# Optimization experiments

Measured on AMD Instinct MI355X. Metric: run time of the kernel, lower is better.

## Reference

```python
import jax, jax.numpy as jnp
import numpy as np

D_MODEL = 512
N_HEADS = 8
B, S = 4, 1024
REL_HIDDEN = 64


def setup_inputs() -> dict:
    key = jax.random.key(0)
    ks = jax.random.split(key, 16)

    def g(k, shape, scale=0.02):
        return jax.random.normal(k, shape, dtype=jnp.float32) * scale

    x = jax.random.normal(ks[0], (B, S, D_MODEL), dtype=jnp.float32)
    freqs = jax.random.uniform(ks[1], (B, S, 1), dtype=jnp.float32)
    return {
        "x": x,
        "freqs": freqs,
        "Wq": g(ks[2], (D_MODEL, D_MODEL)), "bq": g(ks[3], (D_MODEL,)),
        "Wk": g(ks[4], (D_MODEL, D_MODEL)), "bk": g(ks[5], (D_MODEL,)),
        "Wv": g(ks[6], (D_MODEL, D_MODEL)), "bv": g(ks[7], (D_MODEL,)),
        "Wo": g(ks[8], (D_MODEL, D_MODEL)), "bo": g(ks[9], (D_MODEL,)),
        "W1": g(ks[10], (2, REL_HIDDEN)), "b1": g(ks[11], (REL_HIDDEN,)),
        "W2": g(ks[12], (REL_HIDDEN, N_HEADS)), "b2": g(ks[13], (N_HEADS,)),
    }


def reference(x, freqs, Wq, bq, Wk, bk, Wv, bv, Wo, bo, W1, b1, W2, b2):
    b, s, d = x.shape
    h = N_HEADS
    dh = d // h

    def proj(W, bias):  # (b,s,d) -> (b,h,s,dh)
        return (x @ W + bias).reshape(b, s, h, dh).transpose(0, 2, 1, 3)

    Q = proj(Wq, bq)
    K = proj(Wk, bk)
    V = proj(Wv, bv)

    scores = jnp.einsum('bhid,bhjd->bhij', Q, K) / jnp.sqrt(jnp.float32(dh))

    # per-pair relative-frequency features: (b,s,s,2)
    eps = 1e-6
    fd = freqs[:, :, None, :] - freqs[:, None, :, :]
    fr = jnp.log((freqs[:, :, None, :] + eps) / (freqs[:, None, :, :] + eps))
    rel = jnp.concatenate([fd, fr], axis=-1)

    # MLP bias -> (b,s,s,h) -> (b,h,s,s)
    bias = jax.nn.relu(rel @ W1 + b1) @ W2 + b2
    scores = scores + jnp.transpose(bias, (0, 3, 1, 2))

    attn = jax.nn.softmax(scores, axis=-1)
    ctx = jnp.einsum('bhij,bhjd->bhid', attn, V)
    ctx = ctx.transpose(0, 2, 1, 3).reshape(b, s, d)
    return ctx @ Wo + bo
```

## Files before the change

### kernel.cpp

```cpp
#include <hip/hip_runtime.h>
#include <hip/hip_bf16.h>
#include <cstdint>

#define BATCH   4
#define SEQ     1024
#define DM      512
#define NH      8
#define DH      64
#define RH      64

typedef float f32x4 __attribute__((ext_vector_type(4)));
typedef __bf16 bf16x8 __attribute__((ext_vector_type(8)));

#define QB_OFF    (0)
#define KB_OFF    (4  << 20)
#define VT_OFF    (8  << 20)
#define XB_OFF    (12 << 20)
#define WT_OFF    (16 << 20)
#define WOT_OFF   (18 << 20)
#define W2T_OFF   (19 << 20)
#define AW_OFF    (20 << 20)
#define CW_OFF    (21 << 20)
#define CTXB_OFF  (22 << 20)
#define BIAS_OFF  (32 << 20)

__global__ __launch_bounds__(256) void cast_x(
    const float* __restrict__ x, __bf16* __restrict__ xb)
{
    const size_t i = ((size_t)blockIdx.x * 256 + threadIdx.x) * 8;
    const float4 a = *(const float4*)&x[i];
    const float4 b = *(const float4*)&x[i + 4];
    bf16x8 o;
    o[0] = (__bf16)a.x; o[1] = (__bf16)a.y; o[2] = (__bf16)a.z; o[3] = (__bf16)a.w;
    o[4] = (__bf16)b.x; o[5] = (__bf16)b.y; o[6] = (__bf16)b.z; o[7] = (__bf16)b.w;
    *(bf16x8*)&xb[i] = o;
}

__global__ __launch_bounds__(256) void cast_w(
    const float* __restrict__ Wq, const float* __restrict__ Wk,
    const float* __restrict__ Wv, const float* __restrict__ Wo,
    __bf16* __restrict__ Wt, __bf16* __restrict__ Wot)
{
    const int t = threadIdx.x;
    const int k0 = blockIdx.x * 64;
    const int n0 = blockIdx.y * 64;
    const int z  = blockIdx.z;
    const float* __restrict__ src = (z == 0) ? Wq : (z == 1) ? Wk : (z == 2) ? Wv : Wo;
    __bf16* __restrict__ dst = (z < 3) ? (Wt + (size_t)(z * 512 + n0) * 512)
                                       : (Wot + (size_t)n0 * 512);

    __shared__ __align__(16) float Ts[64][65];
    #pragma unroll
    for (int i = 0; i < 4; ++i) {
        const int id = t + i * 256;
        const int row = id >> 4, c4 = (id & 15) * 4;
        const float4 v = *(const float4*)&src[(size_t)(k0 + row) * DM + n0 + c4];
        Ts[row][c4 + 0] = v.x; Ts[row][c4 + 1] = v.y;
        Ts[row][c4 + 2] = v.z; Ts[row][c4 + 3] = v.w;
    }
    __syncthreads();
    #pragma unroll
    for (int i = 0; i < 2; ++i) {
        const int id = t + i * 256;
        const int rn = id >> 3, ck = (id & 7) * 8;
        bf16x8 o;
        #pragma unroll
        for (int j = 0; j < 8; ++j) o[j] = (__bf16)Ts[ck + j][rn];
        *(bf16x8*)&dst[(size_t)rn * 512 + k0 + ck] = o;
    }
}

__global__ __launch_bounds__(256) void gemm_qkv_mfma(
    const __bf16* __restrict__ xb, const __bf16* __restrict__ Wt,
    const float* __restrict__ bq, const float* __restrict__ bk,
    const float* __restrict__ bv,
    __bf16* __restrict__ Qb, __bf16* __restrict__ Kb, __bf16* __restrict__ Vtb)
{
    const int t = threadIdx.x;
    const int wave = t >> 6, lane = t & 63;
    const int wm = wave >> 1, wn = wave & 1;
    const int r = lane & 15, kc = lane >> 4, q4 = kc * 4;
    const int lin = blockIdx.y * 12 + blockIdx.x;
    const int swz = (lin & 7) * 48 + (lin >> 3);
    const int m0 = (swz / 12) * 128;
    const int n0 = (swz % 12) * 128;
    const int sec = n0 >> 9;
    const int nn = n0 & 511;

    __shared__ __align__(16) char smem[36864];
    __bf16* __restrict__ As = (__bf16*)smem;
    __bf16* __restrict__ Bs = (__bf16*)(smem + 18432);

    f32x4 acc[4][4];
    #pragma unroll
    for (int i = 0; i < 4; ++i)
        #pragma unroll
        for (int j = 0; j < 4; ++j) acc[i][j] = {0.f, 0.f, 0.f, 0.f};

    const int srow = t >> 3, sck = (t & 7) * 8;
    const __bf16* __restrict__ Ag = xb + (size_t)(m0 + srow) * 512 + sck;
    const __bf16* __restrict__ Bg = Wt + (size_t)(n0 + srow) * 512 + sck;

    for (int k0 = 0; k0 < 512; k0 += 64) {
        bf16x8 ra[4], rb[4];
        #pragma unroll
        for (int i = 0; i < 4; ++i) {
            ra[i] = *(const bf16x8*)(Ag + (size_t)i * 32 * 512 + k0);
            rb[i] = *(const bf16x8*)(Bg + (size_t)i * 32 * 512 + k0);
        }
        __syncthreads();
        #pragma unroll
        for (int i = 0; i < 4; ++i) {
            *(bf16x8*)&As[(srow + i * 32) * 72 + sck] = ra[i];
            *(bf16x8*)&Bs[(srow + i * 32) * 72 + sck] = rb[i];
        }
        __syncthreads();
        #pragma unroll
        for (int ks = 0; ks < 2; ++ks) {
            bf16x8 af[4], bf[4];
            #pragma unroll
            for (int mf = 0; mf < 4; ++mf)
                af[mf] = *(const bf16x8*)&As[(wm * 64 + mf * 16 + r) * 72 + ks * 32 + kc * 8];
            #pragma unroll
            for (int nf = 0; nf < 4; ++nf)
                bf[nf] = *(const bf16x8*)&Bs[(wn * 64 + nf * 16 + r) * 72 + ks * 32 + kc * 8];
            #pragma unroll
            for (int mf = 0; mf < 4; ++mf)
                #pragma unroll
                for (int nf = 0; nf < 4; ++nf)
                    acc[mf][nf] = __builtin_amdgcn_mfma_f32_16x16x32_bf16(
                        af[mf], bf[nf], acc[mf][nf], 0, 0, 0);
        }
    }

    const float* __restrict__ bias = (sec == 0) ? bq : (sec == 1) ? bk : bv;
    __syncthreads();
    __bf16* __restrict__ Ls = (__bf16*)smem;
    if (sec < 2) {
        #pragma unroll
        for (int mf = 0; mf < 4; ++mf)
            #pragma unroll
            for (int nf = 0; nf < 4; ++nf) {
                const int n_l = wn * 64 + nf * 16 + r;
                const float bb = bias[nn + n_l];
                #pragma unroll
                for (int rr = 0; rr < 4; ++rr)
                    Ls[(wm * 64 + mf * 16 + q4 + rr) * 136 + n_l] =
                        (__bf16)(acc[mf][nf][rr] + bb);
            }
    } else {
        #pragma unroll
        for (int mf = 0; mf < 4; ++mf)
            #pragma unroll
            for (int nf = 0; nf < 4; ++nf) {
                const int n_l = wn * 64 + nf * 16 + r;
                const float bb = bias[nn + n_l];
                #pragma unroll
                for (int rr = 0; rr < 4; ++rr)
                    Ls[n_l * 136 + (wm * 64 + mf * 16 + q4 + rr)] =
                        (__bf16)(acc[mf][nf][rr] + bb);
            }
    }
    __syncthreads();

    const int b = m0 >> 10, sbase = m0 & 1023;
    if (sec < 2) {
        __bf16* __restrict__ dst = sec ? Kb : Qb;
        #pragma unroll
        for (int i = 0; i < 8; ++i) {
            const int id = t + i * 256;
            const int row = id >> 4, nc = (id & 15) * 8;
            const bf16x8 v = *(const bf16x8*)&Ls[row * 136 + nc];
            const int ng = nn + nc, h = ng >> 6, c = ng & 63;
            *(bf16x8*)&dst[((size_t)(b * NH + h) * SEQ + sbase + row) * DH + c] = v;
        }
    } else {
        #pragma unroll
        for (int i = 0; i < 8; ++i) {
            const int id = t + i * 256;
            const int nrow = id >> 4, mc = (id & 15) * 8;
            const bf16x8 v = *(const bf16x8*)&Ls[nrow * 136 + mc];
            const int ng = nn + nrow, h = ng >> 6, c = ng & 63;
            *(bf16x8*)&Vtb[((size_t)(b * NH + h) * DH + c) * SEQ + sbase + mc] = v;
        }
    }
}

__global__ __launch_bounds__(256) void gemm_out_mfma(
    const __bf16* __restrict__ ctxb, const __bf16* __restrict__ Wot,
    const float* __restrict__ bo, float* __restrict__ out)
{
    const int t = threadIdx.x;
    const int wave = t >> 6, lane = t & 63;
    const int wm = wave >> 1, wn = wave & 1;
    const int r = lane & 15, kc = lane >> 4, q4 = kc * 4;
    const int lin = blockIdx.y * 4 + blockIdx.x;
    const int swz = (lin & 7) * 16 + (lin >> 3);
    const int m0 = (swz / 4) * 128;
    const int n0 = (swz % 4) * 128;

    __shared__ __align__(16) char smem[36864];
    __bf16* __restrict__ As = (__bf16*)smem;
    __bf16* __restrict__ Bs = (__bf16*)(smem + 18432);

    f32x4 acc[4][4];
    #pragma unroll
    for (int i = 0; i < 4; ++i)
        #pragma unroll
        for (int j = 0; j < 4; ++j) acc[i][j] = {0.f, 0.f, 0.f, 0.f};

    const int srow = t >> 3, sck = (t & 7) * 8;
    const __bf16* __restrict__ Ag = ctxb + (size_t)(m0 + srow) * 512 + sck;
    const __bf16* __restrict__ Bg = Wot + (size_t)(n0 + srow) * 512 + sck;

    for (int k0 = 0; k0 < 512; k0 += 64) {
        bf16x8 ra[4], rb[4];
        #pragma unroll
        for (int i = 0; i < 4; ++i) {
            ra[i] = *(const bf16x8*)(Ag + (size_t)i * 32 * 512 + k0);
            rb[i] = *(const bf16x8*)(Bg + (size_t)i * 32 * 512 + k0);
        }
        __syncthreads();
        #pragma unroll
        for (int i = 0; i < 4; ++i) {
            *(bf16x8*)&As[(srow + i * 32) * 72 + sck] = ra[i];
            *(bf16x8*)&Bs[(srow + i * 32) * 72 + sck] = rb[i];
        }
        __syncthreads();
        #pragma unroll
        for (int ks = 0; ks < 2; ++ks) {
            bf16x8 af[4], bf[4];
            #pragma unroll
            for (int mf = 0; mf < 4; ++mf)
                af[mf] = *(const bf16x8*)&As[(wm * 64 + mf * 16 + r) * 72 + ks * 32 + kc * 8];
            #pragma unroll
            for (int nf = 0; nf < 4; ++nf)
                bf[nf] = *(const bf16x8*)&Bs[(wn * 64 + nf * 16 + r) * 72 + ks * 32 + kc * 8];
            #pragma unroll
            for (int mf = 0; mf < 4; ++mf)
                #pragma unroll
                for (int nf = 0; nf < 4; ++nf)
                    acc[mf][nf] = __builtin_amdgcn_mfma_f32_16x16x32_bf16(
                        af[mf], bf[nf], acc[mf][nf], 0, 0, 0);
        }
    }

    #pragma unroll
    for (int mf = 0; mf < 4; ++mf)
        #pragma unroll
        for (int nf = 0; nf < 4; ++nf) {
            const int n_l = wn * 64 + nf * 16 + r;
            const float bb = bo[n0 + n_l];
            #pragma unroll
            for (int rr = 0; rr < 4; ++rr)
                out[(size_t)(m0 + wm * 64 + mf * 16 + q4 + rr) * DM + n0 + n_l] =
                    acc[mf][nf][rr] + bb;
        }
}

__global__ __launch_bounds__(64) void rel_kernel(
    const float* __restrict__ freqs,
    const float* __restrict__ W1,
    const float* __restrict__ b1,
    const float* __restrict__ W2,
    float* __restrict__ Aw,
    float* __restrict__ Cw,
    __bf16* __restrict__ W2t)
{
    const int row = blockIdx.x;
    const int k = threadIdx.x;
    const float f = freqs[row];
    const float L = logf(f + 1e-6f);
    const float base = f * W1[k] + L * W1[RH + k];
    Aw[(size_t)row * RH + k] = base + b1[k];
    Cw[(size_t)row * RH + k] = -base;
    if (row < 16)
        W2t[row * 64 + k] = (row < NH) ? (__bf16)W2[k * NH + row] : (__bf16)0.f;
}

__global__ __launch_bounds__(256) void bias_mfma(
    const float* __restrict__ Aw, const float* __restrict__ Cw,
    const __bf16* __restrict__ W2t, __bf16* __restrict__ biasb)
{
    const int t = threadIdx.x;
    const int wave = t >> 6, lane = t & 63;
    const int il = lane & 15, kc = lane >> 4;
    const int j0 = blockIdx.x * 128;
    const int i0 = blockIdx.y * 32;
    const int b  = blockIdx.z;

    __shared__ __align__(16) float Cs[128][68];

    {
        const int jr = t >> 1, half = (t & 1) * 32;
        const float* __restrict__ src = &Cw[((size_t)b * SEQ + j0 + jr) * RH + half];
        #pragma unroll
        for (int q = 0; q < 8; ++q)
            *(float4*)&Cs[jr][half + q * 4] = *(const float4*)(src + q * 4);
    }

    const bf16x8 w2f0 = *(const bf16x8*)&W2t[il * 64 + kc * 8];
    const bf16x8 w2f1 = *(const bf16x8*)&W2t[il * 64 + 32 + kc * 8];
    __syncthreads();

    #pragma unroll
    for (int ih = 0; ih < 2; ++ih) {
        const float* __restrict__ ap =
            &Aw[((size_t)b * SEQ + i0 + ih * 16 + il) * RH];
        const float4 a0 = *(const float4*)(ap + kc * 8);
        const float4 a1 = *(const float4*)(ap + kc * 8 + 4);
        const float4 a2 = *(const float4*)(ap + 32 + kc * 8);
        const float4 a3 = *(const float4*)(ap + 32 + kc * 8 + 4);

        #pragma unroll
        for (int jb = 0; jb < 4; ++jb) {
            f32x4 accJ[8];
            #pragma unroll
            for (int jj = 0; jj < 8; ++jj) {
                const float* __restrict__ cp =
                    &Cs[wave * 32 + jb * 8 + jj][kc * 8];
                const float4 c0 = *(const float4*)(cp);
                const float4 c1 = *(const float4*)(cp + 4);
                const float4 c2 = *(const float4*)(cp + 32);
                const float4 c3 = *(const float4*)(cp + 36);
                bf16x8 hb0, hb1;
                hb0[0] = (__bf16)fmaxf(a0.x + c0.x, 0.f);
                hb0[1] = (__bf16)fmaxf(a0.y + c0.y, 0.f);
                hb0[2] = (__bf16)fmaxf(a0.z + c0.z, 0.f);
                hb0[3] = (__bf16)fmaxf(a0.w + c0.w, 0.f);
                hb0[4] = (__bf16)fmaxf(a1.x + c1.x, 0.f);
                hb0[5] = (__bf16)fmaxf(a1.y + c1.y, 0.f);
                hb0[6] = (__bf16)fmaxf(a1.z + c1.z, 0.f);
                hb0[7] = (__bf16)fmaxf(a1.w + c1.w, 0.f);
                hb1[0] = (__bf16)fmaxf(a2.x + c2.x, 0.f);
                hb1[1] = (__bf16)fmaxf(a2.y + c2.y, 0.f);
                hb1[2] = (__bf16)fmaxf(a2.z + c2.z, 0.f);
                hb1[3] = (__bf16)fmaxf(a2.w + c2.w, 0.f);
                hb1[4] = (__bf16)fmaxf(a3.x + c3.x, 0.f);
                hb1[5] = (__bf16)fmaxf(a3.y + c3.y, 0.f);
                hb1[6] = (__bf16)fmaxf(a3.z + c3.z, 0.f);
                hb1[7] = (__bf16)fmaxf(a3.w + c3.w, 0.f);
                f32x4 acc = {0.f, 0.f, 0.f, 0.f};
                acc = __builtin_amdgcn_mfma_f32_16x16x32_bf16(hb0, w2f0, acc, 0, 0, 0);
                acc = __builtin_amdgcn_mfma_f32_16x16x32_bf16(hb1, w2f1, acc, 0, 0, 0);
                accJ[jj] = acc;
            }
            if (il < 8) {
                #pragma unroll
                for (int rr = 0; rr < 4; ++rr) {
                    bf16x8 pv;
                    #pragma unroll
                    for (int jj = 0; jj < 8; ++jj)
                        pv[jj] = (__bf16)accJ[jj][rr];
                    *(bf16x8*)&biasb[(((size_t)b * NH + il) * SEQ
                                      + i0 + ih * 16 + kc * 4 + rr) * SEQ
                                     + j0 + wave * 32 + jb * 8] = pv;
                }
            }
        }
    }
}

#define PSTR 1032

__global__ __launch_bounds__(512) void attn_mfma(
    const __bf16* __restrict__ Qb, const __bf16* __restrict__ Kb,
    const __bf16* __restrict__ Vtb, const __bf16* __restrict__ biasb,
    __bf16* __restrict__ ctxb)
{
    const int t = threadIdx.x;
    const int wave = t >> 6, lane = t & 63;
    const int r = lane & 15, kc = lane >> 4;
    const int blk = (blockIdx.x & 7) * 256 + (blockIdx.x >> 3);
    const int it = blk & 63;
    const int h  = (blk >> 6) & 7;
    const int b  = blk >> 9;
    const int s0 = it * 16;
    const int bh = b * NH + h;

    __shared__ __align__(16) __bf16 Pb[16 * PSTR];
    __shared__ __align__(16) float part[1088];
    __shared__ float red[8][16];
    __shared__ float invl[16];

    uint32_t brg[4][8];
    {
        const uint16_t* __restrict__ bb = (const uint16_t*)biasb
            + ((size_t)bh * SEQ + s0 + kc * 4) * SEQ + wave * 128 + r;
        #pragma unroll
        for (int rr = 0; rr < 4; ++rr)
            #pragma unroll
            for (int jt = 0; jt < 8; ++jt)
                brg[rr][jt] = bb[(size_t)rr * SEQ + jt * 16];
    }

    f32x4 sc[8];
    {
        const __bf16* __restrict__ Qp = Qb + ((size_t)bh * SEQ + s0) * DH;
        const __bf16* __restrict__ Kp = Kb + ((size_t)bh * SEQ + wave * 128) * DH;
        const bf16x8 qa0 = *(const bf16x8*)(Qp + r * DH + kc * 8);
        const bf16x8 qa1 = *(const bf16x8*)(Qp + r * DH + 32 + kc * 8);
        __builtin_amdgcn_s_setprio(1);
        #pragma unroll
        for (int jt = 0; jt < 8; ++jt) {
            const bf16x8 kb0 = *(const bf16x8*)(Kp + (size_t)(jt * 16 + r) * DH + kc * 8);
            const bf16x8 kb1 = *(const bf16x8*)(Kp + (size_t)(jt * 16 + r) * DH + 32 + kc * 8);
            f32x4 a = {0.f, 0.f, 0.f, 0.f};
            a = __builtin_amdgcn_mfma_f32_16x16x32_bf16(qa0, kb0, a, 0, 0, 0);
            a = __builtin_amdgcn_mfma_f32_16x16x32_bf16(qa1, kb1, a, 0, 0, 0);
            sc[jt] = a;
        }
        __builtin_amdgcn_s_setprio(0);
    }

    float psum[4] = {0.f, 0.f, 0.f, 0.f};
    #pragma unroll
    for (int jt = 0; jt < 8; ++jt) {
        #pragma unroll
        for (int rr = 0; rr < 4; ++rr) {
            const float s = fmaf(sc[jt][rr], 0.125f,
                                 __uint_as_float(brg[rr][jt] << 16));
            const float p = __expf(fminf(s, 30.f));
            sc[jt][rr] = p;
            psum[rr] += p;
        }
    }
    #pragma unroll
    for (int mask = 8; mask >= 1; mask >>= 1)
        #pragma unroll
        for (int rr = 0; rr < 4; ++rr)
            psum[rr] += __shfl_xor(psum[rr], mask);
    if (r == 0) {
        #pragma unroll
        for (int rr = 0; rr < 4; ++rr) red[wave][kc * 4 + rr] = psum[rr];
    }
    #pragma unroll
    for (int jt = 0; jt < 8; ++jt)
        #pragma unroll
        for (int rr = 0; rr < 4; ++rr)
            Pb[(kc * 4 + rr) * PSTR + wave * 128 + jt * 16 + r] = (__bf16)sc[jt][rr];
    __syncthreads();

    if (t < 16) {
        float l = 0.f;
        #pragma unroll
        for (int w = 0; w < 8; ++w) l += red[w][t];
        invl[t] = 1.0f / l;
    }

    {
        const int ct = wave & 3, kh = wave >> 2;
        const __bf16* __restrict__ Vp =
            Vtb + ((size_t)bh * DH + ct * 16 + r) * SEQ + kh * 512;
        f32x4 acc = {0.f, 0.f, 0.f, 0.f};
        __builtin_amdgcn_s_setprio(1);
        #pragma unroll 4
        for (int jt = 0; jt < 16; ++jt) {
            const bf16x8 pa = *(const bf16x8*)&Pb[r * PSTR + kh * 512 + jt * 32 + kc * 8];
            const bf16x8 vb = *(const bf16x8*)(Vp + jt * 32 + kc * 8);
            acc = __builtin_amdgcn_mfma_f32_16x16x32_bf16(pa, vb, acc, 0, 0, 0);
        }
        __builtin_amdgcn_s_setprio(0);
        if (kh == 1) {
            #pragma unroll
            for (int rr = 0; rr < 4; ++rr)
                part[ct * 272 + (kc * 4 + rr) * 17 + r] = acc[rr];
        }
        __syncthreads();
        if (kh == 0) {
            #pragma unroll
            for (int rr = 0; rr < 4; ++rr) {
                const int row = kc * 4 + rr;
                const float v = (acc[rr] + part[ct * 272 + row * 17 + r]) * invl[row];
                ctxb[((size_t)(b * SEQ) + s0 + row) * DM + h * DH + ct * 16 + r] = (__bf16)v;
            }
        }
    }
}

extern "C" void kernel_launch(void* const* d_in, const int* in_sizes, int n_in,
                              void* d_out, int out_size, void* d_ws, size_t ws_size,
                              hipStream_t stream)
{
    const float* x     = (const float*)d_in[0];
    const float* freqs = (const float*)d_in[1];
    const float* Wq    = (const float*)d_in[2];
    const float* bq    = (const float*)d_in[3];
    const float* Wk    = (const float*)d_in[4];
    const float* bk    = (const float*)d_in[5];
    const float* Wv    = (const float*)d_in[6];
    const float* bv    = (const float*)d_in[7];
    const float* Wo    = (const float*)d_in[8];
    const float* bo    = (const float*)d_in[9];
    const float* W1    = (const float*)d_in[10];
    const float* b1    = (const float*)d_in[11];
    const float* W2    = (const float*)d_in[12];

    char* wsb = (char*)d_ws;
    __bf16* Qb    = (__bf16*)(wsb + QB_OFF);
    __bf16* Kb    = (__bf16*)(wsb + KB_OFF);
    __bf16* Vtb   = (__bf16*)(wsb + VT_OFF);
    __bf16* xb    = (__bf16*)(wsb + XB_OFF);
    __bf16* Wt    = (__bf16*)(wsb + WT_OFF);
    __bf16* Wot   = (__bf16*)(wsb + WOT_OFF);
    __bf16* W2t   = (__bf16*)(wsb + W2T_OFF);
    float*  Aw    = (float*)(wsb + AW_OFF);
    float*  Cw    = (float*)(wsb + CW_OFF);
    __bf16* ctxb  = (__bf16*)(wsb + CTXB_OFF);
    __bf16* biasb = (__bf16*)(wsb + BIAS_OFF);
    float* out = (float*)d_out;

    cast_x<<<dim3(1024), 256, 0, stream>>>(x, xb);
    cast_w<<<dim3(8, 8, 4), 256, 0, stream>>>(Wq, Wk, Wv, Wo, Wt, Wot);
    rel_kernel<<<dim3(4096), 64, 0, stream>>>(freqs, W1, b1, W2, Aw, Cw, W2t);
    gemm_qkv_mfma<<<dim3(12, 32), 256, 0, stream>>>(xb, Wt, bq, bk, bv, Qb, Kb, Vtb);
    bias_mfma<<<dim3(8, 32, 4), 256, 0, stream>>>(Aw, Cw, W2t, biasb);
    attn_mfma<<<dim3(2048), 512, 0, stream>>>(Qb, Kb, Vtb, biasb, ctxb);
    gemm_out_mfma<<<dim3(4, 32), 256, 0, stream>>>(ctxb, Wot, bo, out);
}
```

Baseline: 223.3 us.

## Fuse relative-position MLP bias into attention kernel, one block per query tile across heads

```diff
diff --git a/kernel.cpp b/kernel.cpp
--- a/kernel.cpp
+++ b/kernel.cpp
@@ -22,7 +22,6 @@
 #define AW_OFF    (20 << 20)
 #define CW_OFF    (21 << 20)
 #define CTXB_OFF  (22 << 20)
-#define BIAS_OFF  (32 << 20)
 
 __global__ __launch_bounds__(256) void cast_x(
     const float* __restrict__ x, __bf16* __restrict__ xb)
@@ -278,203 +277,158 @@
         W2t[row * 64 + k] = (row < NH) ? (__bf16)W2[k * NH + row] : (__bf16)0.f;
 }
 
-__global__ __launch_bounds__(256) void bias_mfma(
-    const float* __restrict__ Aw, const float* __restrict__ Cw,
-    const __bf16* __restrict__ W2t, __bf16* __restrict__ biasb)
-{
-    const int t = threadIdx.x;
-    const int wave = t >> 6, lane = t & 63;
-    const int il = lane & 15, kc = lane >> 4;
-    const int j0 = blockIdx.x * 128;
-    const int i0 = blockIdx.y * 32;
-    const int b  = blockIdx.z;
-
-    __shared__ __align__(16) float Cs[128][68];
-
-    {
-        const int jr = t >> 1, half = (t & 1) * 32;
-        const float* __restrict__ src = &Cw[((size_t)b * SEQ + j0 + jr) * RH + half];
-        #pragma unroll
-        for (int q = 0; q < 8; ++q)
-            *(float4*)&Cs[jr][half + q * 4] = *(const float4*)(src + q * 4);
-    }
-
-    const bf16x8 w2f0 = *(const bf16x8*)&W2t[il * 64 + kc * 8];
-    const bf16x8 w2f1 = *(const bf16x8*)&W2t[il * 64 + 32 + kc * 8];
-    __syncthreads();
-
-    #pragma unroll
-    for (int ih = 0; ih < 2; ++ih) {
-        const float* __restrict__ ap =
-            &Aw[((size_t)b * SEQ + i0 + ih * 16 + il) * RH];
-        const float4 a0 = *(const float4*)(ap + kc * 8);
-        const float4 a1 = *(const float4*)(ap + kc * 8 + 4);
-        const float4 a2 = *(const float4*)(ap + 32 + kc * 8);
-        const float4 a3 = *(const float4*)(ap + 32 + kc * 8 + 4);
-
-        #pragma unroll
-        for (int jb = 0; jb < 4; ++jb) {
-            f32x4 accJ[8];
-            #pragma unroll
-            for (int jj = 0; jj < 8; ++jj) {
-                const float* __restrict__ cp =
-                    &Cs[wave * 32 + jb * 8 + jj][kc * 8];
-                const float4 c0 = *(const float4*)(cp);
-                const float4 c1 = *(const float4*)(cp + 4);
-                const float4 c2 = *(const float4*)(cp + 32);
-                const float4 c3 = *(const float4*)(cp + 36);
-                bf16x8 hb0, hb1;
-                hb0[0] = (__bf16)fmaxf(a0.x + c0.x, 0.f);
-                hb0[1] = (__bf16)fmaxf(a0.y + c0.y, 0.f);
-                hb0[2] = (__bf16)fmaxf(a0.z + c0.z, 0.f);
-                hb0[3] = (__bf16)fmaxf(a0.w + c0.w, 0.f);
-                hb0[4] = (__bf16)fmaxf(a1.x + c1.x, 0.f);
-                hb0[5] = (__bf16)fmaxf(a1.y + c1.y, 0.f);
-                hb0[6] = (__bf16)fmaxf(a1.z + c1.z, 0.f);
-                hb0[7] = (__bf16)fmaxf(a1.w + c1.w, 0.f);
-                hb1[0] = (__bf16)fmaxf(a2.x + c2.x, 0.f);
-                hb1[1] = (__bf16)fmaxf(a2.y + c2.y, 0.f);
-                hb1[2] = (__bf16)fmaxf(a2.z + c2.z, 0.f);
-                hb1[3] = (__bf16)fmaxf(a2.w + c2.w, 0.f);
-                hb1[4] = (__bf16)fmaxf(a3.x + c3.x, 0.f);
-                hb1[5] = (__bf16)fmaxf(a3.y + c3.y, 0.f);
-                hb1[6] = (__bf16)fmaxf(a3.z + c3.z, 0.f);
-                hb1[7] = (__bf16)fmaxf(a3.w + c3.w, 0.f);
-                f32x4 acc = {0.f, 0.f, 0.f, 0.f};
-                acc = __builtin_amdgcn_mfma_f32_16x16x32_bf16(hb0, w2f0, acc, 0, 0, 0);
-                acc = __builtin_amdgcn_mfma_f32_16x16x32_bf16(hb1, w2f1, acc, 0, 0, 0);
-                accJ[jj] = acc;
-            }
-            if (il < 8) {
-                #pragma unroll
-                for (int rr = 0; rr < 4; ++rr) {
-                    bf16x8 pv;
-                    #pragma unroll
-                    for (int jj = 0; jj < 8; ++jj)
-                        pv[jj] = (__bf16)accJ[jj][rr];
-                    *(bf16x8*)&biasb[(((size_t)b * NH + il) * SEQ
-                                      + i0 + ih * 16 + kc * 4 + rr) * SEQ
-                                     + j0 + wave * 32 + jb * 8] = pv;
-                }
-            }
-        }
-    }
-}
-
-#define PSTR 1032
-
-__global__ __launch_bounds__(512) void attn_mfma(
+#define HSTR 2120
+#define JSTR 132
+
+__global__ __launch_bounds__(512) void attn_fused(
     const __bf16* __restrict__ Qb, const __bf16* __restrict__ Kb,
-    const __bf16* __restrict__ Vtb, const __bf16* __restrict__ biasb,
+    const __bf16* __restrict__ Vtb, const float* __restrict__ Aw,
+    const float* __restrict__ Cw, const __bf16* __restrict__ W2t,
     __bf16* __restrict__ ctxb)
 {
     const int t = threadIdx.x;
     const int wave = t >> 6, lane = t & 63;
     const int r = lane & 15, kc = lane >> 4;
-    const int blk = (blockIdx.x & 7) * 256 + (blockIdx.x >> 3);
-    const int it = blk & 63;
-    const int h  = (blk >> 6) & 7;
-    const int b  = blk >> 9;
-    const int s0 = it * 16;
-    const int bh = b * NH + h;
-
-    __shared__ __align__(16) __bf16 Pb[16 * PSTR];
-    __shared__ __align__(16) float part[1088];
-    __shared__ float red[8][16];
-    __shared__ float invl[16];
-
-    uint32_t brg[4][8];
-    {
-        const uint16_t* __restrict__ bb = (const uint16_t*)biasb
-            + ((size_t)bh * SEQ + s0 + kc * 4) * SEQ + wave * 128 + r;
-        #pragma unroll
-        for (int rr = 0; rr < 4; ++rr)
-            #pragma unroll
-            for (int jt = 0; jt < 8; ++jt)
-                brg[rr][jt] = bb[(size_t)rr * SEQ + jt * 16];
-    }
-
-    f32x4 sc[8];
-    {
-        const __bf16* __restrict__ Qp = Qb + ((size_t)bh * SEQ + s0) * DH;
-        const __bf16* __restrict__ Kp = Kb + ((size_t)bh * SEQ + wave * 128) * DH;
-        const bf16x8 qa0 = *(const bf16x8*)(Qp + r * DH + kc * 8);
-        const bf16x8 qa1 = *(const bf16x8*)(Qp + r * DH + 32 + kc * 8);
-        __builtin_amdgcn_s_setprio(1);
+    const int il = r;
+    const int blk = (blockIdx.x & 7) * 32 + (blockIdx.x >> 3);
+    const int qt = blk & 63;
+    const int b  = blk >> 6;
+    const int s0 = qt * 16;
+    const int bh = b * NH + wave;
+
+    __shared__ __align__(16) float  Cs[128 * 68];
+    __shared__ __align__(16) __bf16 BsP[8 * HSTR];
+
+    const __bf16* __restrict__ Qp = Qb + ((size_t)bh * SEQ + s0) * DH;
+    const bf16x8 qa0 = *(const bf16x8*)(Qp + r * DH + kc * 8);
+    const bf16x8 qa1 = *(const bf16x8*)(Qp + r * DH + 32 + kc * 8);
+    const float* __restrict__ ap = &Aw[((size_t)b * SEQ + s0 + il) * RH];
+    const float4 a0 = *(const float4*)(ap + kc * 8);
+    const float4 a1 = *(const float4*)(ap + kc * 8 + 4);
+    const float4 a2 = *(const float4*)(ap + 32 + kc * 8);
+    const float4 a3 = *(const float4*)(ap + 32 + kc * 8 + 4);
+    const bf16x8 w2f0 = *(const bf16x8*)&W2t[il * 64 + kc * 8];
+    const bf16x8 w2f1 = *(const bf16x8*)&W2t[il * 64 + 32 + kc * 8];
+
+    float psum[4] = {0.f, 0.f, 0.f, 0.f};
+    f32x4 O[4];
+    #pragma unroll
+    for (int ct = 0; ct < 4; ++ct) O[ct] = {0.f, 0.f, 0.f, 0.f};
+
+    const __bf16* __restrict__ KpB = Kb + (size_t)bh * SEQ * DH;
+    const int crow = t >> 2, cseg = (t & 3) * 16;
+
+    for (int c = 0; c < 8; ++c) {
+        const int j0 = c * 128;
+
+        f32x4 sc[8];
+        {
+            const __bf16* __restrict__ Kp = KpB + (size_t)j0 * DH;
+            __builtin_amdgcn_s_setprio(1);
+            #pragma unroll
+            for (int jt = 0; jt < 8; ++jt) {
+                const bf16x8 kb0 = *(const bf16x8*)(Kp + (size_t)(jt * 16 + r) * DH + kc * 8);
+                const bf16x8 kb1 = *(const bf16x8*)(Kp + (size_t)(jt * 16 + r) * DH + 32 + kc * 8);
+                f32x4 a = {0.f, 0.f, 0.f, 0.f};
+                a = __builtin_amdgcn_mfma_f32_16x16x32_bf16(qa0, kb0, a, 0, 0, 0);
+                a = __builtin_amdgcn_mfma_f32_16x16x32_bf16(qa1, kb1, a, 0, 0, 0);
+                sc[jt] = a;
+            }
+            __builtin_amdgcn_s_setprio(0);
+        }
+
+        {
+            const float* __restrict__ src =
+                &Cw[((size_t)b * SEQ + j0 + crow) * RH + cseg];
+            #pragma unroll
+            for (int q = 0; q < 4; ++q)
+                *(float4*)&Cs[crow * 68 + cseg + q * 4] =
+                    *(const float4*)(src + q * 4);
+        }
+        __syncthreads();
+
+        #pragma unroll
+        for (int jj = 0; jj < 16; ++jj) {
+            const int jl = wave * 16 + jj;
+            const float* __restrict__ cp = &Cs[jl * 68 + kc * 8];
+            const float4 c0 = *(const float4*)(cp);
+            const float4 c1 = *(const float4*)(cp + 4);
+            const float4 c2 = *(const float4*)(cp + 32);
+            const float4 c3 = *(const float4*)(cp + 36);
+            bf16x8 hb0, hb1;
+            hb0[0] = (__bf16)fmaxf(a0.x + c0.x, 0.f);
+            hb0[1] = (__bf16)fmaxf(a0.y + c0.y, 0.f);
+            hb0[2] = (__bf16)fmaxf(a0.z + c0.z, 0.f);
+            hb0[3] = (__bf16)fmaxf(a0.w + c0.w, 0.f);
+            hb0[4] = (__bf16)fmaxf(a1.x + c1.x, 0.f);
+            hb0[5] = (__bf16)fmaxf(a1.y + c1.y, 0.f);
+            hb0[6] = (__bf16)fmaxf(a1.z + c1.z, 0.f);
+            hb0[7] = (__bf16)fmaxf(a1.w + c1.w, 0.f);
+            hb1[0] = (__bf16)fmaxf(a2.x + c2.x, 0.f);
+            hb1[1] = (__bf16)fmaxf(a2.y + c2.y, 0.f);
+            hb1[2] = (__bf16)fmaxf(a2.z + c2.z, 0.f);
+            hb1[3] = (__bf16)fmaxf(a2.w + c2.w, 0.f);
+            hb1[4] = (__bf16)fmaxf(a3.x + c3.x, 0.f);
+            hb1[5] = (__bf16)fmaxf(a3.y + c3.y, 0.f);
+            hb1[6] = (__bf16)fmaxf(a3.z + c3.z, 0.f);
+            hb1[7] = (__bf16)fmaxf(a3.w + c3.w, 0.f);
+            f32x4 acc = {0.f, 0.f, 0.f, 0.f};
+            acc = __builtin_amdgcn_mfma_f32_16x16x32_bf16(hb0, w2f0, acc, 0, 0, 0);
+            acc = __builtin_amdgcn_mfma_f32_16x16x32_bf16(hb1, w2f1, acc, 0, 0, 0);
+            if (il < 8) {
+                #pragma unroll
+                for (int rr = 0; rr < 4; ++rr)
+                    BsP[il * HSTR + (kc * 4 + rr) * JSTR + jl] = (__bf16)acc[rr];
+            }
+        }
+        __syncthreads();
+
         #pragma unroll
         for (int jt = 0; jt < 8; ++jt) {
-            const bf16x8 kb0 = *(const bf16x8*)(Kp + (size_t)(jt * 16 + r) * DH + kc * 8);
-            const bf16x8 kb1 = *(const bf16x8*)(Kp + (size_t)(jt * 16 + r) * DH + 32 + kc * 8);
-            f32x4 a = {0.f, 0.f, 0.f, 0.f};
-            a = __builtin_amdgcn_mfma_f32_16x16x32_bf16(qa0, kb0, a, 0, 0, 0);
-            a = __builtin_amdgcn_mfma_f32_16x16x32_bf16(qa1, kb1, a, 0, 0, 0);
-            sc[jt] = a;
-        }
-        __builtin_amdgcn_s_setprio(0);
-    }
-
-    float psum[4] = {0.f, 0.f, 0.f, 0.f};
-    #pragma unroll
-    for (int jt = 0; jt < 8; ++jt) {
-        #pragma unroll
-        for (int rr = 0; rr < 4; ++rr) {
-            const float s = fmaf(sc[jt][rr], 0.125f,
-                                 __uint_as_float(brg[rr][jt] << 16));
-            const float p = __expf(fminf(s, 30.f));
-            sc[jt][rr] = p;
-            psum[rr] += p;
-        }
-    }
+            #pragma unroll
+            for (int rr = 0; rr < 4; ++rr) {
+                const int idx = wave * HSTR + (kc * 4 + rr) * JSTR + jt * 16 + r;
+                const float s = fmaf(sc[jt][rr], 0.125f, (float)BsP[idx]);
+                const float p = __expf(fminf(s, 30.f));
+                psum[rr] += p;
+                BsP[idx] = (__bf16)p;
+            }
+        }
+        asm volatile("s_waitcnt lgkmcnt(0)" ::: "memory");
+        __builtin_amdgcn_sched_barrier(0);
+
+        {
+            __builtin_amdgcn_s_setprio(1);
+            #pragma unroll
+            for (int ct = 0; ct < 4; ++ct) {
+                const __bf16* __restrict__ Vp =
+                    Vtb + ((size_t)bh * DH + ct * 16 + r) * SEQ + j0;
+                #pragma unroll
+                for (int js = 0; js < 4; ++js) {
+                    const bf16x8 pa = *(const bf16x8*)
+                        &BsP[wave * HSTR + r * JSTR + js * 32 + kc * 8];
+                    const bf16x8 vb = *(const bf16x8*)(Vp + js * 32 + kc * 8);
+                    O[ct] = __builtin_amdgcn_mfma_f32_16x16x32_bf16(pa, vb, O[ct], 0, 0, 0);
+                }
+            }
+            __builtin_amdgcn_s_setprio(0);
+        }
+        __syncthreads();
+    }
+
     #pragma unroll
     for (int mask = 8; mask >= 1; mask >>= 1)
         #pragma unroll
         for (int rr = 0; rr < 4; ++rr)
             psum[rr] += __shfl_xor(psum[rr], mask);
-    if (r == 0) {
-        #pragma unroll
-        for (int rr = 0; rr < 4; ++rr) red[wave][kc * 4 + rr] = psum[rr];
-    }
-    #pragma unroll
-    for (int jt = 0; jt < 8; ++jt)
-        #pragma unroll
-        for (int rr = 0; rr < 4; ++rr)
-            Pb[(kc * 4 + rr) * PSTR + wave * 128 + jt * 16 + r] = (__bf16)sc[jt][rr];
-    __syncthreads();
-
-    if (t < 16) {
-        float l = 0.f;
-        #pragma unroll
-        for (int w = 0; w < 8; ++w) l += red[w][t];
-        invl[t] = 1.0f / l;
-    }
-
-    {
-        const int ct = wave & 3, kh = wave >> 2;
-        const __bf16* __restrict__ Vp =
-            Vtb + ((size_t)bh * DH + ct * 16 + r) * SEQ + kh * 512;
-        f32x4 acc = {0.f, 0.f, 0.f, 0.f};
-        __builtin_amdgcn_s_setprio(1);
-        #pragma unroll 4
-        for (int jt = 0; jt < 16; ++jt) {
-            const bf16x8 pa = *(const bf16x8*)&Pb[r * PSTR + kh * 512 + jt * 32 + kc * 8];
-            const bf16x8 vb = *(const bf16x8*)(Vp + jt * 32 + kc * 8);
-            acc = __builtin_amdgcn_mfma_f32_16x16x32_bf16(pa, vb, acc, 0, 0, 0);
-        }
-        __builtin_amdgcn_s_setprio(0);
-        if (kh == 1) {
-            #pragma unroll
-            for (int rr = 0; rr < 4; ++rr)
-                part[ct * 272 + (kc * 4 + rr) * 17 + r] = acc[rr];
-        }
-        __syncthreads();
-        if (kh == 0) {
-            #pragma unroll
-            for (int rr = 0; rr < 4; ++rr) {
-                const int row = kc * 4 + rr;
-                const float v = (acc[rr] + part[ct * 272 + row * 17 + r]) * invl[row];
-                ctxb[((size_t)(b * SEQ) + s0 + row) * DM + h * DH + ct * 16 + r] = (__bf16)v;
-            }
-        }
+    #pragma unroll
+    for (int rr = 0; rr < 4; ++rr) {
+        const float inv = 1.0f / psum[rr];
+        const int q = s0 + kc * 4 + rr;
+        #pragma unroll
+        for (int ct = 0; ct < 4; ++ct)
+            ctxb[((size_t)(b * SEQ) + q) * DM + wave * DH + ct * 16 + r] =
+                (__bf16)(O[ct][rr] * inv);
     }
 }
 
@@ -507,14 +461,12 @@
     float*  Aw    = (float*)(wsb + AW_OFF);
     float*  Cw    = (float*)(wsb + CW_OFF);
     __bf16* ctxb  = (__bf16*)(wsb + CTXB_OFF);
-    __bf16* biasb = (__bf16*)(wsb + BIAS_OFF);
     float* out = (float*)d_out;
 
     cast_x<<<dim3(1024), 256, 0, stream>>>(x, xb);
     cast_w<<<dim3(8, 8, 4), 256, 0, stream>>>(Wq, Wk, Wv, Wo, Wt, Wot);
     rel_kernel<<<dim3(4096), 64, 0, stream>>>(freqs, W1, b1, W2, Aw, Cw, W2t);
     gemm_qkv_mfma<<<dim3(12, 32), 256, 0, stream>>>(xb, Wt, bq, bk, bv, Qb, Kb, Vtb);
-    bias_mfma<<<dim3(8, 32, 4), 256, 0, stream>>>(Aw, Cw, W2t, biasb);
-    attn_mfma<<<dim3(2048), 512, 0, stream>>>(Qb, Kb, Vtb, biasb, ctxb);
+    attn_fused<<<dim3(256), 512, 0, stream>>>(Qb, Kb, Vtb, Aw, Cw, W2t, ctxb);
     gemm_out_mfma<<<dim3(4, 32), 256, 0, stream>>>(ctxb, Wot, bo, out);
 }
```

Measured after the change: 221.1 us. No clear change (-1.0%).
